# Kernel tuning notes

Hardware: AMD Instinct MI355X
Metric: run time of the kernel (lower is better)

The kernel has to match this reference:

```python
import jax, jax.numpy as jnp
import numpy as np

B, R, C, DK, RK = 128, 512, 81, 64, 10  # outer batch, ROI_batch, num_classes+1, d_k, r_k


def setup_inputs() -> dict:
    key = jax.random.key(0)
    ks = jax.random.split(key, 6)
    sc = 1.0 / np.sqrt(C).astype(np.float32)
    return {
        "x": jax.random.normal(ks[0], (B * R, C), jnp.float32),
        "Wq": jax.random.normal(ks[1], (C, DK), jnp.float32) * sc,
        "bq": jnp.zeros((DK,), jnp.float32),
        "Wk": jax.random.normal(ks[2], (C, DK), jnp.float32) * sc,
        "bk": jnp.zeros((DK,), jnp.float32),
        "Wfc": jax.random.normal(ks[3], (C, C), jnp.float32) * sc,
        "bfc": jnp.zeros((C,), jnp.float32),
        "prior_rel": jax.random.uniform(ks[4], (C, C), jnp.float32),
    }


def reference(x, Wq, bq, Wk, bk, Wfc, bfc, prior_rel):
    xb = x.reshape(-1, R, C)                                   # [B,R,C]
    q = xb @ Wq + bq                                            # [B,R,DK]
    k = xb @ Wk + bk                                            # [B,R,DK]
    att = jax.nn.softmax(
        jnp.einsum("bid,bjd->bij", q, k) / jnp.sqrt(jnp.float32(DK)), axis=2
    )                                                           # [B,R,R]
    label = jnp.argmax(xb, axis=2)                              # [B,R]; values in [0,C-1], so the li==C skip in the torch code is dead
    vals, idx = jax.lax.top_k(att, RK)                          # [B,R,K]
    bidx = jnp.arange(xb.shape[0])[:, None, None]               # [B,1,1]
    lj = label[bidx, idx]                                       # [B,R,K] label of neighbor j
    li = label[:, :, None]                                      # [B,R,1]
    x_jl = xb[bidx, idx, lj]                                    # [B,R,K] x[b,j,lj]
    contrib = jnp.where(li != lj, prior_rel[lj, li] * vals * x_jl, 0.0)
    iidx = jnp.arange(R)[None, :, None]
    r = jnp.zeros_like(xb).at[bidx, iidx, lj].add(contrib)      # scatter-add into class slot lj
    out = jax.nn.sigmoid(jax.nn.relu(r) @ Wfc + bfc)
    return out.reshape(-1, C)
```

## Files before the change

kernel.cpp:

```cpp
#include <hip/hip_runtime.h>
#include <math.h>
#include <stdint.h>

#define NB 128
#define NR 512
#define NC 81
#define NDK 64
#define NROWS (NB * NR)
#define LOG2E 1.44269504088896340736f

typedef __attribute__((ext_vector_type(8))) short short8v;
typedef __attribute__((ext_vector_type(4))) float float4v;

static __device__ __forceinline__ uint32_t f32_to_bf16_rne(float f) {
    uint32_t u = __float_as_uint(f);
    return (u + 0x7FFFu + ((u >> 16) & 1u)) >> 16;
}

__global__ __launch_bounds__(256) void qk_label_kernel(
    const float* __restrict__ x,
    const float* __restrict__ Wq, const float* __restrict__ bq,
    const float* __restrict__ Wk, const float* __restrict__ bk,
    ushort* __restrict__ Qh, ushort* __restrict__ Ql,
    ushort* __restrict__ Kh, ushort* __restrict__ Kl,
    int* __restrict__ label, float* __restrict__ xmax)
{
    __shared__ float xS[64][84];

    const int t = threadIdx.x;
    const int r0 = blockIdx.x * 64;

#pragma unroll
    for (int k = 0; k < 21; ++k) {
        int flat = t + 256 * k;
        if (flat < 64 * 81) {
            int rr = (int)(((unsigned)flat * 6473u) >> 19);
            int cc = flat - 81 * rr;
            xS[rr][cc] = x[(size_t)r0 * NC + flat];
        }
    }
    __syncthreads();

    if (t < 64) {
        float bv = -INFINITY; int bi = 0;
        for (int c = 0; c < 81; ++c) {
            float v = xS[t][c];
            if (v > bv) { bv = v; bi = c; }
        }
        label[r0 + t] = bi;
        xmax[r0 + t] = bv;
    }

    const int d4 = t & 31;
    const int rgrp = t >> 5;
    const bool isQ = d4 < 16;
    const int ocol = (isQ ? d4 : d4 - 16) * 4;
    const float* Wbase = (isQ ? Wq : Wk) + ocol;

    float acc[8][4];
#pragma unroll
    for (int i = 0; i < 8; ++i)
#pragma unroll
        for (int k = 0; k < 4; ++k) acc[i][k] = 0.f;

#pragma unroll 2
    for (int c4 = 0; c4 < 20; ++c4) {
        const float4 wv0 = *reinterpret_cast<const float4*>(&Wbase[(c4 * 4 + 0) * NDK]);
        const float4 wv1 = *reinterpret_cast<const float4*>(&Wbase[(c4 * 4 + 1) * NDK]);
        const float4 wv2 = *reinterpret_cast<const float4*>(&Wbase[(c4 * 4 + 2) * NDK]);
        const float4 wv3 = *reinterpret_cast<const float4*>(&Wbase[(c4 * 4 + 3) * NDK]);
#pragma unroll
        for (int i = 0; i < 8; ++i) {
            const float4 xv = *reinterpret_cast<const float4*>(&xS[rgrp * 8 + i][c4 * 4]);
            acc[i][0] = fmaf(xv.x, wv0.x, acc[i][0]);
            acc[i][1] = fmaf(xv.x, wv0.y, acc[i][1]);
            acc[i][2] = fmaf(xv.x, wv0.z, acc[i][2]);
            acc[i][3] = fmaf(xv.x, wv0.w, acc[i][3]);
            acc[i][0] = fmaf(xv.y, wv1.x, acc[i][0]);
            acc[i][1] = fmaf(xv.y, wv1.y, acc[i][1]);
            acc[i][2] = fmaf(xv.y, wv1.z, acc[i][2]);
            acc[i][3] = fmaf(xv.y, wv1.w, acc[i][3]);
            acc[i][0] = fmaf(xv.z, wv2.x, acc[i][0]);
            acc[i][1] = fmaf(xv.z, wv2.y, acc[i][1]);
            acc[i][2] = fmaf(xv.z, wv2.z, acc[i][2]);
            acc[i][3] = fmaf(xv.z, wv2.w, acc[i][3]);
            acc[i][0] = fmaf(xv.w, wv3.x, acc[i][0]);
            acc[i][1] = fmaf(xv.w, wv3.y, acc[i][1]);
            acc[i][2] = fmaf(xv.w, wv3.z, acc[i][2]);
            acc[i][3] = fmaf(xv.w, wv3.w, acc[i][3]);
        }
    }
    {
        const float4 wv = *reinterpret_cast<const float4*>(&Wbase[80 * NDK]);
#pragma unroll
        for (int i = 0; i < 8; ++i) {
            const float xv = xS[rgrp * 8 + i][80];
            acc[i][0] = fmaf(xv, wv.x, acc[i][0]);
            acc[i][1] = fmaf(xv, wv.y, acc[i][1]);
            acc[i][2] = fmaf(xv, wv.z, acc[i][2]);
            acc[i][3] = fmaf(xv, wv.w, acc[i][3]);
        }
    }

    const float* bias = isQ ? bq : bk;
    const float b0 = bias[ocol + 0], b1 = bias[ocol + 1];
    const float b2 = bias[ocol + 2], b3 = bias[ocol + 3];
    ushort* Hi = isQ ? Qh : Kh;
    ushort* Lo = isQ ? Ql : Kl;
    const int kc = ocol >> 3;
    const int sub = ocol & 7;
    const int bb = r0 >> 9;
    const int rl0 = (r0 & 511) + rgrp * 8;

#pragma unroll
    for (int i = 0; i < 8; ++i) {
        float z0 = acc[i][0] + b0, z1 = acc[i][1] + b1;
        float z2 = acc[i][2] + b2, z3 = acc[i][3] + b3;
        uint32_t h0 = f32_to_bf16_rne(z0), h1 = f32_to_bf16_rne(z1);
        uint32_t h2 = f32_to_bf16_rne(z2), h3 = f32_to_bf16_rne(z3);
        uint32_t l0 = f32_to_bf16_rne(z0 - __uint_as_float(h0 << 16));
        uint32_t l1 = f32_to_bf16_rne(z1 - __uint_as_float(h1 << 16));
        uint32_t l2 = f32_to_bf16_rne(z2 - __uint_as_float(h2 << 16));
        uint32_t l3 = f32_to_bf16_rne(z3 - __uint_as_float(h3 << 16));
        size_t base = (((size_t)bb * 8 + kc) * 512 + rl0 + i) * 8 + sub;
        uint2 hv; hv.x = h0 | (h1 << 16); hv.y = h2 | (h3 << 16);
        uint2 lv; lv.x = l0 | (l1 << 16); lv.y = l2 | (l3 << 16);
        *reinterpret_cast<uint2*>(&Hi[base]) = hv;
        *reinterpret_cast<uint2*>(&Lo[base]) = lv;
    }
}

__global__ __launch_bounds__(256, 4) void attn_kernel(
    const ushort* __restrict__ Qh, const ushort* __restrict__ Ql,
    const ushort* __restrict__ Kh, const ushort* __restrict__ Kl,
    const int* __restrict__ label, const float* __restrict__ xmax,
    const float* __restrict__ Wfc, const float* __restrict__ bfc,
    const float* __restrict__ prior, float* __restrict__ out)
{
    __shared__ float WfcS[NC * NC];
    __shared__ float bfcS[NC];
    __shared__ int   labS[NR];
    __shared__ float xmS[NR];
    __shared__ float fcv[64][10];
    __shared__ int   flj[64][10];

    const int t = threadIdx.x;
    const int b  = blockIdx.x & 127;
    const int ig = blockIdx.x >> 7;
    const int lane = t & 63;
    const int wv = t >> 6;
    const int lr = lane & 15;
    const int lq = lane >> 4;

    for (int e = t; e < NC * NC; e += 256) WfcS[e] = Wfc[e];
    if (t < NC) bfcS[t] = bfc[t];
    for (int e = t; e < NR; e += 256) {
        labS[e] = label[b * NR + e];
        xmS[e]  = xmax[b * NR + e];
    }

    const int i = ig * 64 + wv * 16 + lr;

    short8v qh[2], ql[2];
#pragma unroll
    for (int ks = 0; ks < 2; ++ks) {
        size_t qoff = (((size_t)b * 8 + ks * 4 + lq) * 512 + i) * 8;
        qh[ks] = *reinterpret_cast<const short8v*>(&Qh[qoff]);
        ql[ks] = *reinterpret_cast<const short8v*>(&Ql[qoff]);
    }

    __syncthreads();

    uint32_t tv[10];
#pragma unroll
    for (int s = 0; s < 10; ++s) tv[s] = 0u;
    float lsum = 0.f;

    const ushort* kh0 = &Kh[(((size_t)b * 8 + 0 * 4 + lq) * 512 + lr) * 8];
    const ushort* kh1 = &Kh[(((size_t)b * 8 + 1 * 4 + lq) * 512 + lr) * 8];
    const ushort* kl0 = &Kl[(((size_t)b * 8 + 0 * 4 + lq) * 512 + lr) * 8];
    const ushort* kl1 = &Kl[(((size_t)b * 8 + 1 * 4 + lq) * 512 + lr) * 8];

#pragma unroll 2
    for (int jt = 0; jt < 32; ++jt) {
        float4v c = {0.f, 0.f, 0.f, 0.f};
        {
            short8v ah0 = *reinterpret_cast<const short8v*>(kh0 + jt * 128);
            short8v al0 = *reinterpret_cast<const short8v*>(kl0 + jt * 128);
            c = __builtin_amdgcn_mfma_f32_16x16x32_bf16(ah0, qh[0], c, 0, 0, 0);
            c = __builtin_amdgcn_mfma_f32_16x16x32_bf16(al0, qh[0], c, 0, 0, 0);
            c = __builtin_amdgcn_mfma_f32_16x16x32_bf16(ah0, ql[0], c, 0, 0, 0);
        }
        {
            short8v ah1 = *reinterpret_cast<const short8v*>(kh1 + jt * 128);
            short8v al1 = *reinterpret_cast<const short8v*>(kl1 + jt * 128);
            c = __builtin_amdgcn_mfma_f32_16x16x32_bf16(ah1, qh[1], c, 0, 0, 0);
            c = __builtin_amdgcn_mfma_f32_16x16x32_bf16(al1, qh[1], c, 0, 0, 0);
            c = __builtin_amdgcn_mfma_f32_16x16x32_bf16(ah1, ql[1], c, 0, 0, 0);
        }
        const int jb = jt * 16 + lq * 4;
#pragma unroll
        for (int r2 = 0; r2 < 4; ++r2) {
            const float sc = c[r2] * 0.125f;
            lsum += exp2f(sc * LOG2E);
            uint32_t kb = f32_to_bf16_rne(sc);
            kb ^= (kb & 0x8000u) ? 0xFFFFu : 0x8000u;
            uint32_t p = (kb << 9) | (uint32_t)(511 - (jb + r2));
#pragma unroll
            for (int s = 0; s < 10; ++s) {
                uint32_t hi = tv[s] > p ? tv[s] : p;
                uint32_t lo = tv[s] > p ? p : tv[s];
                tv[s] = hi; p = lo;
            }
        }
    }

#pragma unroll
    for (int m = 16; m <= 32; m <<= 1) {
        lsum += __shfl_xor(lsum, m, 64);
        uint32_t inc[10];
#pragma unroll
        for (int s = 0; s < 10; ++s) inc[s] = __shfl_xor(tv[s], m, 64);
#pragma unroll
        for (int s2 = 0; s2 < 10; ++s2) {
            uint32_t p = inc[s2];
#pragma unroll
            for (int s = 0; s < 10; ++s) {
                uint32_t hi = tv[s] > p ? tv[s] : p;
                uint32_t lo = tv[s] > p ? p : tv[s];
                tv[s] = hi; p = lo;
            }
        }
    }

    if (lq == 0) {
        const float inv = 1.f / lsum;
        const int li = labS[i];
        float cv[10]; int lj[10];
#pragma unroll
        for (int k2 = 0; k2 < 10; ++k2) {
            uint32_t p = tv[k2];
            int j = 511 - (int)(p & 511u);
            uint32_t kb = p >> 9;
            uint32_t s16 = kb ^ ((kb & 0x8000u) ? 0x8000u : 0xFFFFu);
            float scq = __uint_as_float(s16 << 16);
            float val = exp2f(scq * LOG2E) * inv;
            int l = labS[j];
            cv[k2] = (l != li) ? prior[l * NC + li] * val * xmS[j] : 0.f;
            lj[k2] = l;
        }
#pragma unroll
        for (int a2 = 1; a2 < 10; ++a2)
#pragma unroll
            for (int b2 = 0; b2 < a2; ++b2)
                if (lj[a2] == lj[b2]) { cv[b2] += cv[a2]; cv[a2] = 0.f; break; }
#pragma unroll
        for (int k2 = 0; k2 < 10; ++k2) cv[k2] = fmaxf(cv[k2], 0.f);

        const int rowInBlk = wv * 16 + lr;
#pragma unroll
        for (int k2 = 0; k2 < 10; ++k2) {
            fcv[rowInBlk][k2] = cv[k2];
            flj[rowInBlk][k2] = lj[k2];
        }
    }
    __syncthreads();

    {
        const int erow = t >> 2;
        const int cq = t & 3;
        const size_t eg = (size_t)(b * NR + ig * 64 + erow) * NC;
        float ecv[10]; int elj[10];
#pragma unroll
        for (int s = 0; s < 10; ++s) { ecv[s] = fcv[erow][s]; elj[s] = flj[erow][s]; }
        for (int c = cq; c < NC; c += 4) {
            float z = bfcS[c];
#pragma unroll
            for (int k2 = 0; k2 < 10; ++k2)
                z = fmaf(ecv[k2], WfcS[elj[k2] * NC + c], z);
            out[eg + c] = 1.f / (1.f + exp2f(-z * LOG2E));
        }
    }
}

extern "C" void kernel_launch(void* const* d_in, const int* in_sizes, int n_in,
                              void* d_out, int out_size, void* d_ws, size_t ws_size,
                              hipStream_t stream)
{
    const float* x     = (const float*)d_in[0];
    const float* Wq    = (const float*)d_in[1];
    const float* bq    = (const float*)d_in[2];
    const float* Wk    = (const float*)d_in[3];
    const float* bk    = (const float*)d_in[4];
    const float* Wfc   = (const float*)d_in[5];
    const float* bfc   = (const float*)d_in[6];
    const float* prior = (const float*)d_in[7];
    float* out = (float*)d_out;

    ushort* Qh = (ushort*)d_ws;
    ushort* Ql = Qh + (size_t)NROWS * NDK;
    ushort* Kh = Ql + (size_t)NROWS * NDK;
    ushort* Kl = Kh + (size_t)NROWS * NDK;
    int*   label = (int*)(Kl + (size_t)NROWS * NDK);
    float* xmax  = (float*)(label + NROWS);

    qk_label_kernel<<<NROWS / 64, 256, 0, stream>>>(
        x, Wq, bq, Wk, bk, Qh, Ql, Kh, Kl, label, xmax);

    attn_kernel<<<1024, 256, 0, stream>>>(
        Qh, Ql, Kh, Kl, label, xmax, Wfc, bfc, prior, out);
}
```

Baseline: 171.9 us.

## Stage Q/K bf16 splits in LDS for coalesced stores; streamline top-k insertion

The QK projection kernel now writes its hi/lo bf16 outputs into a shared-memory buffer that aliases the x tile, then copies them out in contiguous uint2 chunks. The aim is coalesced global writes in place of scattered 8-byte stores. The attention loop splits the MFMA accumulation into two independent chains, uses a shorter min/max top-10 insertion network, and applies the 1/8 scale after keying so the sort key no longer needs a multiply. Fast intrinsics (__expf, __fdividef) replace exp2f and exact division, at some cost in accuracy. The extra syncthreads and LDS round trip add some overhead to the first kernel.

```diff
diff --git a/kernel.cpp b/kernel.cpp
--- a/kernel.cpp
+++ b/kernel.cpp
@@ -7,7 +7,6 @@
 #define NC 81
 #define NDK 64
 #define NROWS (NB * NR)
-#define LOG2E 1.44269504088896340736f
 
 typedef __attribute__((ext_vector_type(8))) short short8v;
 typedef __attribute__((ext_vector_type(4))) float float4v;
@@ -25,7 +24,10 @@
     ushort* __restrict__ Kh, ushort* __restrict__ Kl,
     int* __restrict__ label, float* __restrict__ xmax)
 {
-    __shared__ float xS[64][84];
+    __shared__ union {
+        float  xS[64][84];
+        ushort pk[4][8][520];
+    } uA;
 
     const int t = threadIdx.x;
     const int r0 = blockIdx.x * 64;
@@ -36,7 +38,7 @@
         if (flat < 64 * 81) {
             int rr = (int)(((unsigned)flat * 6473u) >> 19);
             int cc = flat - 81 * rr;
-            xS[rr][cc] = x[(size_t)r0 * NC + flat];
+            uA.xS[rr][cc] = x[(size_t)r0 * NC + flat];
         }
     }
     __syncthreads();
@@ -44,7 +46,7 @@
     if (t < 64) {
         float bv = -INFINITY; int bi = 0;
         for (int c = 0; c < 81; ++c) {
-            float v = xS[t][c];
+            float v = uA.xS[t][c];
             if (v > bv) { bv = v; bi = c; }
         }
         label[r0 + t] = bi;
@@ -71,7 +73,7 @@
         const float4 wv3 = *reinterpret_cast<const float4*>(&Wbase[(c4 * 4 + 3) * NDK]);
 #pragma unroll
         for (int i = 0; i < 8; ++i) {
-            const float4 xv = *reinterpret_cast<const float4*>(&xS[rgrp * 8 + i][c4 * 4]);
+            const float4 xv = *reinterpret_cast<const float4*>(&uA.xS[rgrp * 8 + i][c4 * 4]);
             acc[i][0] = fmaf(xv.x, wv0.x, acc[i][0]);
             acc[i][1] = fmaf(xv.x, wv0.y, acc[i][1]);
             acc[i][2] = fmaf(xv.x, wv0.z, acc[i][2]);
@@ -94,7 +96,7 @@
         const float4 wv = *reinterpret_cast<const float4*>(&Wbase[80 * NDK]);
 #pragma unroll
         for (int i = 0; i < 8; ++i) {
-            const float xv = xS[rgrp * 8 + i][80];
+            const float xv = uA.xS[rgrp * 8 + i][80];
             acc[i][0] = fmaf(xv, wv.x, acc[i][0]);
             acc[i][1] = fmaf(xv, wv.y, acc[i][1]);
             acc[i][2] = fmaf(xv, wv.z, acc[i][2]);
@@ -105,12 +107,11 @@
     const float* bias = isQ ? bq : bk;
     const float b0 = bias[ocol + 0], b1 = bias[ocol + 1];
     const float b2 = bias[ocol + 2], b3 = bias[ocol + 3];
-    ushort* Hi = isQ ? Qh : Kh;
-    ushort* Lo = isQ ? Ql : Kl;
+    const int aH = isQ ? 0 : 2;
     const int kc = ocol >> 3;
     const int sub = ocol & 7;
-    const int bb = r0 >> 9;
-    const int rl0 = (r0 & 511) + rgrp * 8;
+
+    __syncthreads();
 
 #pragma unroll
     for (int i = 0; i < 8; ++i) {
@@ -122,11 +123,24 @@
         uint32_t l1 = f32_to_bf16_rne(z1 - __uint_as_float(h1 << 16));
         uint32_t l2 = f32_to_bf16_rne(z2 - __uint_as_float(h2 << 16));
         uint32_t l3 = f32_to_bf16_rne(z3 - __uint_as_float(h3 << 16));
-        size_t base = (((size_t)bb * 8 + kc) * 512 + rl0 + i) * 8 + sub;
         uint2 hv; hv.x = h0 | (h1 << 16); hv.y = h2 | (h3 << 16);
         uint2 lv; lv.x = l0 | (l1 << 16); lv.y = l2 | (l3 << 16);
-        *reinterpret_cast<uint2*>(&Hi[base]) = hv;
-        *reinterpret_cast<uint2*>(&Lo[base]) = lv;
+        const int lofs = (rgrp * 8 + i) * 8 + sub;
+        *reinterpret_cast<uint2*>(&uA.pk[aH][kc][lofs])     = hv;
+        *reinterpret_cast<uint2*>(&uA.pk[aH + 1][kc][lofs]) = lv;
+    }
+    __syncthreads();
+
+    const int bb = r0 >> 9;
+    const int rl0 = r0 & 511;
+#pragma unroll
+    for (int m = 0; m < 16; ++m) {
+        int F = t + 256 * m;
+        int a = F >> 10, rem = F & 1023;
+        int kc2 = rem >> 7, f4 = rem & 127;
+        uint2 v = *reinterpret_cast<const uint2*>(&uA.pk[a][kc2][f4 * 4]);
+        ushort* dst = (a == 0) ? Qh : (a == 1) ? Ql : (a == 2) ? Kh : Kl;
+        *(reinterpret_cast<uint2*>(dst + (((size_t)bb * 8 + kc2) * 512 + rl0) * 8) + f4) = v;
     }
 }
 
@@ -175,6 +189,7 @@
 #pragma unroll
     for (int s = 0; s < 10; ++s) tv[s] = 0u;
     float lsum = 0.f;
+    const int invb = 511 - lq * 4;
 
     const ushort* kh0 = &Kh[(((size_t)b * 8 + 0 * 4 + lq) * 512 + lr) * 8];
     const ushort* kh1 = &Kh[(((size_t)b * 8 + 1 * 4 + lq) * 512 + lr) * 8];
@@ -183,35 +198,38 @@
 
 #pragma unroll 2
     for (int jt = 0; jt < 32; ++jt) {
-        float4v c = {0.f, 0.f, 0.f, 0.f};
+        float4v ca = {0.f, 0.f, 0.f, 0.f};
+        float4v cb = {0.f, 0.f, 0.f, 0.f};
         {
             short8v ah0 = *reinterpret_cast<const short8v*>(kh0 + jt * 128);
             short8v al0 = *reinterpret_cast<const short8v*>(kl0 + jt * 128);
-            c = __builtin_amdgcn_mfma_f32_16x16x32_bf16(ah0, qh[0], c, 0, 0, 0);
-            c = __builtin_amdgcn_mfma_f32_16x16x32_bf16(al0, qh[0], c, 0, 0, 0);
-            c = __builtin_amdgcn_mfma_f32_16x16x32_bf16(ah0, ql[0], c, 0, 0, 0);
+            ca = __builtin_amdgcn_mfma_f32_16x16x32_bf16(ah0, qh[0], ca, 0, 0, 0);
+            ca = __builtin_amdgcn_mfma_f32_16x16x32_bf16(al0, qh[0], ca, 0, 0, 0);
+            ca = __builtin_amdgcn_mfma_f32_16x16x32_bf16(ah0, ql[0], ca, 0, 0, 0);
         }
         {
             short8v ah1 = *reinterpret_cast<const short8v*>(kh1 + jt * 128);
             short8v al1 = *reinterpret_cast<const short8v*>(kl1 + jt * 128);
-            c = __builtin_amdgcn_mfma_f32_16x16x32_bf16(ah1, qh[1], c, 0, 0, 0);
-            c = __builtin_amdgcn_mfma_f32_16x16x32_bf16(al1, qh[1], c, 0, 0, 0);
-            c = __builtin_amdgcn_mfma_f32_16x16x32_bf16(ah1, ql[1], c, 0, 0, 0);
-        }
-        const int jb = jt * 16 + lq * 4;
+            cb = __builtin_amdgcn_mfma_f32_16x16x32_bf16(ah1, qh[1], cb, 0, 0, 0);
+            cb = __builtin_amdgcn_mfma_f32_16x16x32_bf16(al1, qh[1], cb, 0, 0, 0);
+            cb = __builtin_amdgcn_mfma_f32_16x16x32_bf16(ah1, ql[1], cb, 0, 0, 0);
+        }
+        const int invt = invb - jt * 16;
 #pragma unroll
         for (int r2 = 0; r2 < 4; ++r2) {
-            const float sc = c[r2] * 0.125f;
-            lsum += exp2f(sc * LOG2E);
-            uint32_t kb = f32_to_bf16_rne(sc);
-            kb ^= (kb & 0x8000u) ? 0xFFFFu : 0x8000u;
-            uint32_t p = (kb << 9) | (uint32_t)(511 - (jb + r2));
-#pragma unroll
-            for (int s = 0; s < 10; ++s) {
-                uint32_t hi = tv[s] > p ? tv[s] : p;
-                uint32_t lo = tv[s] > p ? p : tv[s];
-                tv[s] = hi; p = lo;
+            const float cf = ca[r2] + cb[r2];
+            lsum += __expf(cf * 0.125f);
+            uint32_t u = __float_as_uint(cf);
+            uint32_t sgn = (uint32_t)((int32_t)u >> 31);
+            uint32_t k32 = u ^ (sgn | 0x80000000u);
+            uint32_t kb = (k32 + 0x7FFFu + ((k32 >> 16) & 1u)) >> 16;
+            uint32_t p = (kb << 9) | (uint32_t)(invt - r2);
+#pragma unroll
+            for (int s = 9; s >= 1; --s) {
+                uint32_t mn = tv[s - 1] < p ? tv[s - 1] : p;
+                tv[s] = tv[s] > mn ? tv[s] : mn;
             }
+            tv[0] = tv[0] > p ? tv[0] : p;
         }
     }
 
@@ -225,16 +243,16 @@
         for (int s2 = 0; s2 < 10; ++s2) {
             uint32_t p = inc[s2];
 #pragma unroll
-            for (int s = 0; s < 10; ++s) {
-                uint32_t hi = tv[s] > p ? tv[s] : p;
-                uint32_t lo = tv[s] > p ? p : tv[s];
-                tv[s] = hi; p = lo;
+            for (int s = 9; s >= 1; --s) {
+                uint32_t mn = tv[s - 1] < p ? tv[s - 1] : p;
+                tv[s] = tv[s] > mn ? tv[s] : mn;
             }
+            tv[0] = tv[0] > p ? tv[0] : p;
         }
     }
 
     if (lq == 0) {
-        const float inv = 1.f / lsum;
+        const float inv = __fdividef(1.f, lsum);
         const int li = labS[i];
         float cv[10]; int lj[10];
 #pragma unroll
@@ -242,9 +260,9 @@
             uint32_t p = tv[k2];
             int j = 511 - (int)(p & 511u);
             uint32_t kb = p >> 9;
-            uint32_t s16 = kb ^ ((kb & 0x8000u) ? 0x8000u : 0xFFFFu);
+            uint32_t s16 = (kb & 0x8000u) ? (kb ^ 0x8000u) : (kb ^ 0xFFFFu);
             float scq = __uint_as_float(s16 << 16);
-            float val = exp2f(scq * LOG2E) * inv;
+            float val = __expf(scq * 0.125f) * inv;
             int l = labS[j];
             cv[k2] = (l != li) ? prior[l * NC + li] * val * xmS[j] : 0.f;
             lj[k2] = l;
@@ -278,7 +296,7 @@
 #pragma unroll
             for (int k2 = 0; k2 < 10; ++k2)
                 z = fmaf(ecv[k2], WfcS[elj[k2] * NC + c], z);
-            out[eg + c] = 1.f / (1.f + exp2f(-z * LOG2E));
+            out[eg + c] = __fdividef(1.f, 1.f + __expf(-z));
         }
     }
 }
```

Measured after the change: 161.0 us. -6.3%, faster.
